# Performance work log

Hardware: AMD Instinct MI355X
Metric: run time of the kernel (lower is better)

## Reference

```python
import jax, jax.numpy as jnp
import numpy as np

RY = jnp.array([[-1.0, 0.0, 0.0], [0.0, 1.0, 0.0], [0.0, 0.0, -1.0]], dtype=jnp.float32)


def quat2mat(q):
    # q: [N,4] -> [N,3,3], same formula as the torch quaternion2matrix (no normalization)
    q0, q1, q2, q3 = q[:, 0], q[:, 1], q[:, 2], q[:, 3]
    r0 = jnp.stack([q0*q0 + q1*q1 - q2*q2 - q3*q3, 2*(q1*q2 - q0*q3), 2*(q1*q3 + q0*q2)], axis=-1)
    r1 = jnp.stack([2*(q1*q2 + q0*q3), q0*q0 - q1*q1 + q2*q2 - q3*q3, 2*(q2*q3 - q0*q1)], axis=-1)
    r2 = jnp.stack([2*(q1*q3 - q0*q2), 2*(q2*q3 + q0*q1), q0*q0 - q1*q1 - q2*q2 + q3*q3], axis=-1)
    return jnp.stack([r0, r1, r2], axis=-2)


def setup_inputs() -> dict:
    key = jax.random.key(0)
    k1, k2, k3, k4, k5, k6 = jax.random.split(key, 6)
    B, H, W, N = 256, 256, 256, 8192
    return {
        "confidence": jax.random.normal(k1, (B, 1, H, W), dtype=jnp.float32),
        "confidence_gt": jax.random.normal(k2, (B, 1, H, W), dtype=jnp.float32),
        "weight": jax.random.uniform(k3, (B, H, W), dtype=jnp.float32),
        "depth_and_rotation": jax.random.normal(k4, (N, 5), dtype=jnp.float32),
        "ann_values": jax.random.normal(k5, (N, 5), dtype=jnp.float32),
        "ann_flags": jax.random.randint(k6, (N,), 0, 2).astype(bool),
    }


def reference(confidence, confidence_gt, weight, depth_and_rotation, ann_values, ann_flags):
    # confidence loss
    diff = confidence[:, 0, ...] - confidence_gt[:, 0, ...]
    confidence_loss = jnp.sum(weight * diff * diff) / (256.0 * 256.0)

    N = ann_values.shape[0]
    mask = ann_flags.astype(jnp.float32)  # [N]

    # depth loss
    d_err = (depth_and_rotation[:, 0] - ann_values[:, 0]) ** 2
    depth_loss = jnp.sum(mask * d_err) / N

    # rotation loss: gt matrix from raw quaternion (unnormalized, as in original),
    # pred matrix from normalized predicted quaternion
    m_pred = quat2mat(ann_values[:, 1:])                      # [N,3,3]
    q = depth_and_rotation[:, 1:]
    q = q / jnp.linalg.norm(q, axis=-1, keepdims=True)
    m_gt = quat2mat(q)                                        # [N,3,3]
    n1 = jnp.linalg.norm((m_gt - m_pred).reshape(N, 9), axis=-1)
    m_pred_ry = jnp.einsum('nij,jk->nik', m_pred, RY)
    n2 = jnp.linalg.norm((m_gt - m_pred_ry).reshape(N, 9), axis=-1)
    rotation_loss = jnp.sum(mask * jnp.minimum(n1, n2)) / N

    return (confidence_loss, depth_loss, rotation_loss)
```

## Files before the change

### kernel.cpp

```cpp
#include <hip/hip_runtime.h>

#define NBLOCKS 4096
#define NTHREADS 256

__device__ __forceinline__ float wave_reduce_sum(float v) {
#pragma unroll
    for (int off = 32; off > 0; off >>= 1)
        v += __shfl_down(v, off, 64);
    return v;
}

__device__ __forceinline__ void quat2mat(float q0, float q1, float q2, float q3,
                                         float m[9]) {
    float q00 = q0 * q0, q11 = q1 * q1, q22 = q2 * q2, q33 = q3 * q3;
    m[0] = q00 + q11 - q22 - q33;
    m[1] = 2.0f * (q1 * q2 - q0 * q3);
    m[2] = 2.0f * (q1 * q3 + q0 * q2);
    m[3] = 2.0f * (q1 * q2 + q0 * q3);
    m[4] = q00 - q11 + q22 - q33;
    m[5] = 2.0f * (q2 * q3 - q0 * q1);
    m[6] = 2.0f * (q1 * q3 - q0 * q2);
    m[7] = 2.0f * (q2 * q3 + q0 * q1);
    m[8] = q00 - q11 - q22 + q33;
}

__device__ __forceinline__ void block_reduce3(float c, float d, float r,
                                              float* dst) {
    c = wave_reduce_sum(c);
    d = wave_reduce_sum(d);
    r = wave_reduce_sum(r);
    __shared__ float s_c[NTHREADS / 64], s_d[NTHREADS / 64], s_r[NTHREADS / 64];
    const int lane = threadIdx.x & 63;
    const int wid = threadIdx.x >> 6;
    if (lane == 0) {
        s_c[wid] = c;
        s_d[wid] = d;
        s_r[wid] = r;
    }
    __syncthreads();
    if (threadIdx.x == 0) {
        float tc = 0.0f, td = 0.0f, tr = 0.0f;
#pragma unroll
        for (int w = 0; w < NTHREADS / 64; ++w) {
            tc += s_c[w];
            td += s_d[w];
            tr += s_r[w];
        }
        dst[0] = tc;
        dst[1] = td;
        dst[2] = tr;
    }
}

__device__ __forceinline__ float wsq(float4 c, float4 g, float4 w) {
    float d0 = c.x - g.x, d1 = c.y - g.y, d2 = c.z - g.z, d3 = c.w - g.w;
    return w.x * d0 * d0 + w.y * d1 * d1 + w.z * d2 * d2 + w.w * d3 * d3;
}

__global__ __launch_bounds__(NTHREADS, 2) void hpnet_partial_kernel(
    const float* __restrict__ conf, const float* __restrict__ conf_gt,
    const float* __restrict__ weight, const float* __restrict__ dr,
    const float* __restrict__ ann, const int* __restrict__ flags,
    float* __restrict__ part,
    long long n_conf, int N) {
    const long long gid = (long long)blockIdx.x * blockDim.x + threadIdx.x;
    const long long S = (long long)NBLOCKS * NTHREADS;

    const float4* __restrict__ c4 = (const float4*)conf;
    const float4* __restrict__ g4 = (const float4*)conf_gt;
    const float4* __restrict__ w4 = (const float4*)weight;
    const long long n4 = n_conf >> 2;

    float acc_c = 0.0f;
    if (gid + 3 * S < n4) {
        float4 c0 = c4[gid];
        float4 c1 = c4[gid + S];
        float4 c2 = c4[gid + 2 * S];
        float4 c3 = c4[gid + 3 * S];
        float4 g0 = g4[gid];
        float4 g1 = g4[gid + S];
        float4 g2 = g4[gid + 2 * S];
        float4 g3 = g4[gid + 3 * S];
        float4 w0 = w4[gid];
        float4 w1 = w4[gid + S];
        float4 w2 = w4[gid + 2 * S];
        float4 w3 = w4[gid + 3 * S];
        acc_c = (wsq(c0, g0, w0) + wsq(c1, g1, w1)) +
                (wsq(c2, g2, w2) + wsq(c3, g3, w3));
    } else {
        for (long long i = gid; i < n4; i += S) acc_c += wsq(c4[i], g4[i], w4[i]);
    }

    float acc_d = 0.0f;
    float acc_r = 0.0f;
    if (gid < N) {
        const long long n = gid;
        float m = flags[n] ? 1.0f : 0.0f;

        float de = dr[n * 5 + 0] - ann[n * 5 + 0];
        acc_d = m * de * de;

        float mp[9];
        quat2mat(ann[n * 5 + 1], ann[n * 5 + 2], ann[n * 5 + 3],
                 ann[n * 5 + 4], mp);

        float p0 = dr[n * 5 + 1], p1 = dr[n * 5 + 2], p2 = dr[n * 5 + 3],
              p3 = dr[n * 5 + 4];
        float inv = 1.0f / sqrtf(p0 * p0 + p1 * p1 + p2 * p2 + p3 * p3);
        float mg[9];
        quat2mat(p0 * inv, p1 * inv, p2 * inv, p3 * inv, mg);

        float s1 = 0.0f, s2 = 0.0f;
#pragma unroll
        for (int r = 0; r < 3; ++r) {
            float a0 = mg[r * 3 + 0], a1 = mg[r * 3 + 1], a2 = mg[r * 3 + 2];
            float b0 = mp[r * 3 + 0], b1 = mp[r * 3 + 1], b2 = mp[r * 3 + 2];
            float e0 = a0 - b0, e1 = a1 - b1, e2 = a2 - b2;
            s1 += e0 * e0 + e1 * e1 + e2 * e2;
            float f0 = a0 + b0, f2 = a2 + b2;
            s2 += f0 * f0 + e1 * e1 + f2 * f2;
        }
        acc_r = m * fminf(sqrtf(s1), sqrtf(s2));
    }

    block_reduce3(acc_c, acc_d, acc_r, &part[3 * blockIdx.x]);
}

__global__ __launch_bounds__(NTHREADS) void hpnet_final_kernel(
    const float* __restrict__ part,
    float* __restrict__ out) {
    float tc = 0.0f, td = 0.0f, tr = 0.0f;
    for (int i = threadIdx.x; i < NBLOCKS; i += NTHREADS) {
        tc += part[3 * i + 0];
        td += part[3 * i + 1];
        tr += part[3 * i + 2];
    }
    __shared__ float dst[3];
    block_reduce3(tc, td, tr, dst);
    __syncthreads();
    if (threadIdx.x == 0) {
        out[0] = dst[0] * (1.0f / (256.0f * 256.0f));
        out[1] = dst[1] * (1.0f / 8192.0f);
        out[2] = dst[2] * (1.0f / 8192.0f);
    }
}

extern "C" void kernel_launch(void* const* d_in, const int* in_sizes, int n_in,
                              void* d_out, int out_size, void* d_ws,
                              size_t ws_size, hipStream_t stream) {
    const float* conf    = (const float*)d_in[0];
    const float* conf_gt = (const float*)d_in[1];
    const float* weight  = (const float*)d_in[2];
    const float* dr      = (const float*)d_in[3];
    const float* ann     = (const float*)d_in[4];
    const int*   flags   = (const int*)d_in[5];
    float* out = (float*)d_out;
    float* part = (float*)d_ws;

    const long long n_conf = (long long)in_sizes[0];
    const int N = in_sizes[5];

    hpnet_partial_kernel<<<NBLOCKS, NTHREADS, 0, stream>>>(
        conf, conf_gt, weight, dr, ann, flags, part, n_conf, N);
    hpnet_final_kernel<<<1, NTHREADS, 0, stream>>>(part, out);
}
```

Measured before the change: 211.7 us.

## Use contiguous per-block chunks with a software-pipelined prefetch loop

```diff
diff --git a/kernel.cpp b/kernel.cpp
--- a/kernel.cpp
+++ b/kernel.cpp
@@ -1,6 +1,6 @@
 #include <hip/hip_runtime.h>
 
-#define NBLOCKS 4096
+#define NBLOCKS 2048
 #define NTHREADS 256
 
 __device__ __forceinline__ float wave_reduce_sum(float v) {
@@ -57,14 +57,13 @@
     return w.x * d0 * d0 + w.y * d1 * d1 + w.z * d2 * d2 + w.w * d3 * d3;
 }
 
-__global__ __launch_bounds__(NTHREADS, 2) void hpnet_partial_kernel(
+__global__ __launch_bounds__(NTHREADS, 4) void hpnet_partial_kernel(
     const float* __restrict__ conf, const float* __restrict__ conf_gt,
     const float* __restrict__ weight, const float* __restrict__ dr,
     const float* __restrict__ ann, const int* __restrict__ flags,
     float* __restrict__ part,
     long long n_conf, int N) {
     const long long gid = (long long)blockIdx.x * blockDim.x + threadIdx.x;
-    const long long S = (long long)NBLOCKS * NTHREADS;
 
     const float4* __restrict__ c4 = (const float4*)conf;
     const float4* __restrict__ g4 = (const float4*)conf_gt;
@@ -72,23 +71,31 @@
     const long long n4 = n_conf >> 2;
 
     float acc_c = 0.0f;
-    if (gid + 3 * S < n4) {
-        float4 c0 = c4[gid];
-        float4 c1 = c4[gid + S];
-        float4 c2 = c4[gid + 2 * S];
-        float4 c3 = c4[gid + 3 * S];
-        float4 g0 = g4[gid];
-        float4 g1 = g4[gid + S];
-        float4 g2 = g4[gid + 2 * S];
-        float4 g3 = g4[gid + 3 * S];
-        float4 w0 = w4[gid];
-        float4 w1 = w4[gid + S];
-        float4 w2 = w4[gid + 2 * S];
-        float4 w3 = w4[gid + 3 * S];
-        acc_c = (wsq(c0, g0, w0) + wsq(c1, g1, w1)) +
-                (wsq(c2, g2, w2) + wsq(c3, g3, w3));
+    if ((n4 % ((long long)NBLOCKS * NTHREADS)) == 0) {
+        const long long chunk = n4 / NBLOCKS;
+        const long long base = (long long)blockIdx.x * chunk + threadIdx.x;
+        const int K = (int)(chunk / NTHREADS);
+
+        float4 c0 = c4[base], g0 = g4[base], w0 = w4[base];
+        float4 c1 = c4[base + NTHREADS], g1 = g4[base + NTHREADS],
+               w1 = w4[base + NTHREADS];
+#pragma unroll 1
+        for (int k = 0; k + 2 < K; ++k) {
+            const long long idx = base + (long long)(k + 2) * NTHREADS;
+            float4 c2 = c4[idx];
+            float4 g2 = g4[idx];
+            float4 w2 = w4[idx];
+            __builtin_amdgcn_sched_barrier(0);
+            acc_c += wsq(c0, g0, w0);
+            c0 = c1; g0 = g1; w0 = w1;
+            c1 = c2; g1 = g2; w1 = w2;
+        }
+        acc_c += wsq(c0, g0, w0);
+        acc_c += wsq(c1, g1, w1);
     } else {
-        for (long long i = gid; i < n4; i += S) acc_c += wsq(c4[i], g4[i], w4[i]);
+        const long long S = (long long)NBLOCKS * NTHREADS;
+        for (long long i = gid; i < n4; i += S)
+            acc_c += wsq(c4[i], g4[i], w4[i]);
     }
 
     float acc_d = 0.0f;
```

After: 202.5 us. -4.3%, faster.
